# Optimization experiments

Measured on AMD Instinct MI355X. Metric: run time of the kernel, lower is better.

Reference implementation:

```python
import jax, jax.numpy as jnp
import numpy as np

EMB = 512
H = 8
DK = EMB // H          # 64
MAX_SEQ = 768
TOPK = MAX_SEQ // 2    # 384


def setup_inputs() -> dict:
    key = jax.random.key(0)
    ks = jax.random.split(key, 16)
    B, S, E = 1, MAX_SEQ, EMB

    def w(k, shape):
        return jax.random.normal(k, shape, dtype=jnp.float32) * 0.02

    return {
        "x": jax.random.normal(ks[0], (B, S, E), dtype=jnp.float32),
        # main attention projections (Linear weights stored as (in, out))
        "Wq": w(ks[1], (E, E)), "bq": w(ks[2], (E,)),
        "Wk": w(ks[3], (E, E)), "bk": w(ks[4], (E,)),
        "Wv": w(ks[5], (E, E)), "bv": w(ks[6], (E,)),
        "Wo": w(ks[7], (E, E)), "bo": w(ks[8], (E,)),
        # indexer projections: wq -> (E, H*DK)=(E,E), wk -> (E, DK), weights_proj -> (E, H)
        "iq_W": w(ks[9], (E, H * DK)), "iq_b": w(ks[10], (H * DK,)),
        "ik_W": w(ks[11], (E, DK)),    "ik_b": w(ks[12], (DK,)),
        "wp_W": w(ks[13], (E, H)),     "wp_b": w(ks[14], (H,)),
    }


def reference(x, Wq, bq, Wk, bk, Wv, bv, Wo, bo, iq_W, iq_b, ik_W, ik_b, wp_W, wp_b):
    B, S, E = x.shape
    scaling = 1.0 / np.sqrt(DK)

    def split_heads(z):  # (B,S,E) -> (B,H,S,DK)
        return z.reshape(B, S, H, DK).transpose(0, 2, 1, 3)

    Q = split_heads(x @ Wq + bq)
    K = split_heads(x @ Wk + bk)
    V = split_heads(x @ Wv + bv)

    # --- indexer: per-token relevance scores ---
    q_idx = (x @ iq_W + iq_b).reshape(B, S, H, DK).transpose(0, 2, 1, 3)  # (B,H,S,DK)
    k_idx = x @ ik_W + ik_b                                               # (B,S,DK)
    w_idx = x @ wp_W + wp_b                                               # (B,S,H)
    score = jax.nn.relu(jnp.einsum('bhsd,btd->bhst', q_idx, k_idx))       # (B,H,S,S)
    indexer_score = jnp.einsum('bhst,bsh->bst', score, w_idx)             # (B,S,S)

    # --- top-k selection (set-equivalent to argpartition in the original) ---
    topk_idx = jax.lax.top_k(indexer_score, TOPK)[1]                      # (B,S,TOPK) int32

    # --- gather sparse K/V per query token ---
    def gather_b(Zb, idxb):  # Zb:(H,S,DK), idxb:(S,TOPK) -> (H,S,TOPK,DK)
        return Zb[:, idxb, :]
    K_s = jax.vmap(gather_b)(K, topk_idx)  # (B,H,S,TOPK,DK)
    V_s = jax.vmap(gather_b)(V, topk_idx)  # (B,H,S,TOPK,DK)

    # --- sparse attention over selected tokens ---
    sc = jnp.einsum('bhsd,bhskd->bhsk', Q, K_s) * scaling  # (B,H,S,TOPK)
    wts = jax.nn.softmax(sc, axis=-1)
    attn = jnp.einsum('bhsk,bhskd->bhsd', wts, V_s)        # (B,H,S,DK)

    out = attn.transpose(0, 2, 1, 3).reshape(B, S, E) @ Wo + bo
    return out
```

## Files before the change

### kernel.cpp

```cpp
#include <hip/hip_runtime.h>
#include <hip/hip_bf16.h>
#include <math.h>

#define S 768
#define E 512
#define H 8
#define DK 64
#define TOPK 384

typedef short bf16x8 __attribute__((ext_vector_type(8)));
typedef float f32x4 __attribute__((ext_vector_type(4)));

__device__ __forceinline__ unsigned short f2bf(float x) {
  unsigned u = __float_as_uint(x);
  unsigned r = u + 0x7FFFu + ((u >> 16) & 1u);
  return (unsigned short)(r >> 16);
}
__device__ __forceinline__ float bf2f(unsigned short h) {
  return __uint_as_float(((unsigned)h) << 16);
}
__device__ __forceinline__ void split1(float x, unsigned short& h, unsigned short& l) {
  h = f2bf(x);
  l = f2bf(x - bf2f(h));
}

__device__ __forceinline__ void mfma3(f32x4& d, bf16x8 ah, bf16x8 al,
                                      bf16x8 bh, bf16x8 bl) {
  d = __builtin_amdgcn_mfma_f32_16x16x32_bf16(ah, bh, d, 0, 0, 0);
  d = __builtin_amdgcn_mfma_f32_16x16x32_bf16(ah, bl, d, 0, 0, 0);
  d = __builtin_amdgcn_mfma_f32_16x16x32_bf16(al, bh, d, 0, 0, 0);
}
__device__ __forceinline__ void mfma2(f32x4& d, bf16x8 ah, bf16x8 al, bf16x8 bh) {
  d = __builtin_amdgcn_mfma_f32_16x16x32_bf16(ah, bh, d, 0, 0, 0);
  d = __builtin_amdgcn_mfma_f32_16x16x32_bf16(al, bh, d, 0, 0, 0);
}

__device__ __forceinline__ bf16x8 ldfrag(const unsigned short* p) {
  return *reinterpret_cast<const bf16x8*>(p);
}

struct PrepTab {
  const float* src[8];
  unsigned short* hi[8];
  unsigned short* lo[8];
};

__global__ __launch_bounds__(256) void prep_kernel(PrepTab t) {
  const int seg = blockIdx.z;
  const int rows = (seg == 0) ? 768 : 512;
  const int cols = (seg == 5) ? 64 : ((seg == 6) ? 8 : 512);
  const int tx = (seg == 6) ? 2 : ((cols + 31) >> 5);
  const int ty = rows >> 5;
  if ((int)blockIdx.x >= tx || (int)blockIdx.y >= ty) return;
  const int r0 = blockIdx.y * 32, c0 = blockIdx.x * 32;
  const int tid = threadIdx.x;
  const int rl = tid >> 3, c4 = (tid & 7) << 2;
  const float* src = t.src[seg];
  if (seg == 0) {
    float4 v = *(const float4*)(src + (size_t)(r0 + rl) * cols + c0 + c4);
    unsigned short h[4], l[4];
    split1(v.x, h[0], l[0]); split1(v.y, h[1], l[1]);
    split1(v.z, h[2], l[2]); split1(v.w, h[3], l[3]);
    size_t off = (size_t)(r0 + rl) * cols + c0 + c4;
    *(ushort4*)(t.hi[seg] + off) = make_ushort4(h[0], h[1], h[2], h[3]);
    *(ushort4*)(t.lo[seg] + off) = make_ushort4(l[0], l[1], l[2], l[3]);
  } else {
    __shared__ float ts[32][33];
    #pragma unroll
    for (int j = 0; j < 4; ++j) {
      int c = c4 + j;
      ts[rl][c] = (c0 + c < cols) ? src[(size_t)(r0 + rl) * cols + c0 + c] : 0.0f;
    }
    __syncthreads();
    float v0 = ts[c4 + 0][rl], v1 = ts[c4 + 1][rl];
    float v2 = ts[c4 + 2][rl], v3 = ts[c4 + 3][rl];
    unsigned short h[4], l[4];
    split1(v0, h[0], l[0]); split1(v1, h[1], l[1]);
    split1(v2, h[2], l[2]); split1(v3, h[3], l[3]);
    size_t off = (size_t)(c0 + rl) * 512 + r0 + c4;
    *(ushort4*)(t.hi[seg] + off) = make_ushort4(h[0], h[1], h[2], h[3]);
    *(ushort4*)(t.lo[seg] + off) = make_ushort4(l[0], l[1], l[2], l[3]);
  }
}

struct ProjTab {
  const unsigned short* whi[6];
  const unsigned short* wlo[6];
  const float* bias[6];
};

__global__ __launch_bounds__(256) void proj_mfma_kernel(
    const unsigned short* __restrict__ Xhi, const unsigned short* __restrict__ Xlo,
    ProjTab pt,
    unsigned short* __restrict__ Qhi, unsigned short* __restrict__ Qlo,
    unsigned short* __restrict__ Khi, unsigned short* __restrict__ Klo,
    unsigned short* __restrict__ VThi,
    unsigned short* __restrict__ QIhi, unsigned short* __restrict__ QIlo,
    unsigned short* __restrict__ KIhi, unsigned short* __restrict__ KIlo,
    float* __restrict__ WI) {
  __shared__ __align__(16) unsigned short Ah[64][72];
  __shared__ __align__(16) unsigned short Al[64][72];
  __shared__ __align__(16) unsigned short Bh[64][72];
  __shared__ __align__(16) unsigned short Bl[64][72];
  const int bx = blockIdx.x;
  int seg, nt;
  if (bx < 32) { seg = bx >> 3; nt = bx & 7; }
  else         { seg = 4 + (bx - 32); nt = 0; }
  const int m0 = blockIdx.y * 64;
  const int n0 = nt * 64;
  const int tid = threadIdx.x;
  const int lane = tid & 63;
  const int wave = tid >> 6;
  const int mq = (wave >> 1) << 5;
  const int nq = (wave & 1) << 5;
  const int l15 = lane & 15;
  const int q8 = (lane >> 4) << 3;
  const int q4 = (lane >> 4) << 2;
  const unsigned short* Whi = pt.whi[seg];
  const unsigned short* Wlo = pt.wlo[seg];

  f32x4 acc[2][2] = {};
  for (int cc = 0; cc < 8; ++cc) {
    const int k0 = cc << 6;
    #pragma unroll
    for (int j = 0; j < 2; ++j) {
      const int flat = tid + (j << 8);
      const int mm = flat >> 3;
      const int kc = (flat & 7) << 3;
      const size_t ga = (size_t)(m0 + mm) * 512 + k0 + kc;
      const size_t gb = (size_t)(n0 + mm) * 512 + k0 + kc;
      *(bf16x8*)&Ah[mm][kc] = ldfrag(Xhi + ga);
      *(bf16x8*)&Al[mm][kc] = ldfrag(Xlo + ga);
      *(bf16x8*)&Bh[mm][kc] = ldfrag(Whi + gb);
      *(bf16x8*)&Bl[mm][kc] = ldfrag(Wlo + gb);
    }
    __syncthreads();
    #pragma unroll
    for (int ki = 0; ki < 64; ki += 32) {
      const int kk = ki + q8;
      bf16x8 ah0 = *(const bf16x8*)&Ah[mq + l15][kk];
      bf16x8 al0 = *(const bf16x8*)&Al[mq + l15][kk];
      bf16x8 ah1 = *(const bf16x8*)&Ah[mq + 16 + l15][kk];
      bf16x8 al1 = *(const bf16x8*)&Al[mq + 16 + l15][kk];
      bf16x8 bh0 = *(const bf16x8*)&Bh[nq + l15][kk];
      bf16x8 bl0 = *(const bf16x8*)&Bl[nq + l15][kk];
      bf16x8 bh1 = *(const bf16x8*)&Bh[nq + 16 + l15][kk];
      bf16x8 bl1 = *(const bf16x8*)&Bl[nq + 16 + l15][kk];
      mfma3(acc[0][0], ah0, al0, bh0, bl0);
      mfma3(acc[0][1], ah0, al0, bh1, bl1);
      mfma3(acc[1][0], ah1, al1, bh0, bl0);
      mfma3(acc[1][1], ah1, al1, bh1, bl1);
    }
    __syncthreads();
  }

  const float* bias = pt.bias[seg];
  #pragma unroll
  for (int ntt = 0; ntt < 2; ++ntt) {
    const int nloc = n0 + nq + ntt * 16 + l15;
    const float bv = (seg == 5 && nloc >= 8) ? 0.0f : bias[nloc];
    #pragma unroll
    for (int mt = 0; mt < 2; ++mt) {
      #pragma unroll
      for (int r = 0; r < 4; ++r) {
        const int m = m0 + mq + mt * 16 + q4 + r;
        const float v = acc[mt][ntt][r] + bv;
        unsigned short h16, l16;
        if (seg == 0) {
          split1(v, h16, l16);
          Qhi[(size_t)m * 512 + nloc] = h16;
          Qlo[(size_t)m * 512 + nloc] = l16;
        } else if (seg == 1) {
          const int hh = nloc >> 6, dd = nloc & 63;
          split1(v, h16, l16);
          Khi[((size_t)hh * S + m) * 64 + dd] = h16;
          Klo[((size_t)hh * S + m) * 64 + dd] = l16;
        } else if (seg == 2) {
          VThi[((size_t)(nloc >> 6) * 64 + (nloc & 63)) * S + m] = f2bf(v);
        } else if (seg == 3) {
          split1(v, h16, l16);
          QIhi[(size_t)m * 512 + nloc] = h16;
          QIlo[(size_t)m * 512 + nloc] = l16;
        } else if (seg == 4) {
          split1(v, h16, l16);
          KIhi[(size_t)m * 64 + nloc] = h16;
          KIlo[(size_t)m * 64 + nloc] = l16;
        } else {
          if (nloc < 8) WI[(size_t)m * 8 + nloc] = v;
        }
      }
    }
  }
}

__global__ __launch_bounds__(512) void indexer_mfma_kernel(
    const unsigned short* __restrict__ QIhi, const unsigned short* __restrict__ QIlo,
    const unsigned short* __restrict__ KIhi, const unsigned short* __restrict__ KIlo,
    const float* __restrict__ WI, float* __restrict__ ISC) {
  __shared__ float wis[32][8];
  __shared__ float AccL[32][65];
  const int s0 = blockIdx.y * 32, t0 = blockIdx.x * 64;
  const int tid512 = threadIdx.x;
  const int z = tid512 >> 8;
  const int tid = tid512 & 255;
  const int lane = tid & 63;
  const int wave = tid >> 6;
  const int mq = (wave >> 1) << 4;
  const int nqb = (wave & 1) << 5;
  const int l15 = lane & 15;
  const int q8 = (lane >> 4) << 3;
  const int q4 = (lane >> 4) << 2;
  if (tid512 < 256) wis[tid512 >> 3][tid512 & 7] = WI[(size_t)(s0 + (tid512 >> 3)) * 8 + (tid512 & 7)];
  __syncthreads();

  const size_t arow = (size_t)(s0 + mq + l15) * 512;
  const size_t brow0 = (size_t)(t0 + nqb + l15) * 64;
  const size_t brow1 = (size_t)(t0 + nqb + 16 + l15) * 64;

  bf16x8 kfh[2][2], kfl[2][2];
  #pragma unroll
  for (int kk = 0; kk < 2; ++kk) {
    const int kb = kk * 32 + q8;
    kfh[kk][0] = ldfrag(KIhi + brow0 + kb);
    kfl[kk][0] = ldfrag(KIlo + brow0 + kb);
    kfh[kk][1] = ldfrag(KIhi + brow1 + kb);
    kfl[kk][1] = ldfrag(KIlo + brow1 + kb);
  }

  float accI[2][4] = {};
  #pragma unroll
  for (int hh = 0; hh < 4; ++hh) {
    const int h = z * 4 + hh;
    f32x4 d[2] = {};
    #pragma unroll
    for (int kk = 0; kk < 2; ++kk) {
      const int ka = h * 64 + kk * 32 + q8;
      bf16x8 ah = ldfrag(QIhi + arow + ka);
      bf16x8 al = ldfrag(QIlo + arow + ka);
      mfma3(d[0], ah, al, kfh[kk][0], kfl[kk][0]);
      mfma3(d[1], ah, al, kfh[kk][1], kfl[kk][1]);
    }
    #pragma unroll
    for (int r = 0; r < 4; ++r) {
      const float w = wis[mq + q4 + r][h];
      accI[0][r] = fmaf(fmaxf(d[0][r], 0.0f), w, accI[0][r]);
      accI[1][r] = fmaf(fmaxf(d[1][r], 0.0f), w, accI[1][r]);
    }
  }
  if (z == 1) {
    #pragma unroll
    for (int ntt = 0; ntt < 2; ++ntt)
      #pragma unroll
      for (int r = 0; r < 4; ++r)
        AccL[mq + q4 + r][nqb + ntt * 16 + l15] = accI[ntt][r];
  }
  __syncthreads();
  if (z == 0) {
    #pragma unroll
    for (int ntt = 0; ntt < 2; ++ntt)
      #pragma unroll
      for (int r = 0; r < 4; ++r)
        ISC[(size_t)(s0 + mq + q4 + r) * S + t0 + nqb + ntt * 16 + l15] =
            accI[ntt][r] + AccL[mq + q4 + r][nqb + ntt * 16 + l15];
  }
}

__global__ __launch_bounds__(256) void topk_kernel(
    const float* __restrict__ ISC, unsigned* __restrict__ Mask,
    float* __restrict__ Sum, float* __restrict__ ATTacc) {
  __shared__ unsigned ordv[768];
  __shared__ int hist[256];
  __shared__ int gsum[16];
  __shared__ int sc[256];
  __shared__ unsigned mw[24];
  __shared__ unsigned sh_prefix;
  __shared__ int sh_R;
  const int s = blockIdx.x;
  const int tid = threadIdx.x;
  for (int i = tid; i < 768; i += 256) {
    float f = ISC[s * 768 + i] + 0.0f;
    unsigned u = __float_as_uint(f);
    ordv[i] = (u & 0x80000000u) ? ~u : (u | 0x80000000u);
  }
  {
    const float4 z4 = {0.0f, 0.0f, 0.0f, 0.0f};
    if (tid < 128) *(float4*)(ATTacc + (size_t)s * 512 + tid * 4) = z4;
  }
  if (tid < 24) mw[tid] = 0u;
  if (tid < H) Sum[tid * S + s] = 0.0f;
  if (tid == 0) { sh_prefix = 0u; sh_R = TOPK; }
  __syncthreads();
  for (int pass = 0; pass < 4; ++pass) {
    const int shift = 24 - pass * 8;
    hist[tid] = 0;
    __syncthreads();
    const unsigned pm = (pass == 0) ? 0u : (0xFFFFFFFFu << (shift + 8));
    const unsigned pref = sh_prefix;
    for (int i = tid; i < 768; i += 256) {
      unsigned o = ordv[i];
      if ((o & pm) == pref) atomicAdd(&hist[(o >> shift) & 255], 1);
    }
    __syncthreads();
    if (tid < 16) {
      int t = 0;
      #pragma unroll
      for (int k = 0; k < 16; ++k) t += hist[tid * 16 + k];
      gsum[tid] = t;
    }
    __syncthreads();
    if (tid == 0) {
      int R = sh_R;
      int G = 0;
      int g = 15;
      for (; g > 0; --g) {
        if (G + gsum[g] >= R) break;
        G += gsum[g];
      }
      int b = 15;
      for (; b > 0; --b) {
        int c = hist[g * 16 + b];
        if (G + c >= R) break;
        G += c;
      }
      sh_prefix = sh_prefix | ((unsigned)(g * 16 + b) << shift);
      sh_R = R - G;
    }
    __syncthreads();
  }
  const unsigned thr = sh_prefix;
  const int need_eq = sh_R;
  const int base = tid * 3;
  unsigned o0 = ordv[base], o1 = ordv[base + 1], o2 = ordv[base + 2];
  int c = (o0 == thr) + (o1 == thr) + (o2 == thr);
  sc[tid] = c;
  __syncthreads();
  for (int off = 1; off < 256; off <<= 1) {
    int v = (tid >= off) ? sc[tid - off] : 0;
    __syncthreads();
    sc[tid] += v;
    __syncthreads();
  }
  int rank = sc[tid] - c;
  if (o0 > thr || (o0 == thr && rank < need_eq))
    atomicOr(&mw[base >> 5], 1u << (base & 31));
  if (o0 == thr) ++rank;
  if (o1 > thr || (o1 == thr && rank < need_eq))
    atomicOr(&mw[(base + 1) >> 5], 1u << ((base + 1) & 31));
  if (o1 == thr) ++rank;
  if (o2 > thr || (o2 == thr && rank < need_eq))
    atomicOr(&mw[(base + 2) >> 5], 1u << ((base + 2) & 31));
  __syncthreads();
  if (tid < 24) Mask[s * 24 + tid] = mw[tid];
}

__global__ __launch_bounds__(256) void sattn_kernel(
    const unsigned short* __restrict__ Qhi, const unsigned short* __restrict__ Qlo,
    const unsigned short* __restrict__ Khi, const unsigned short* __restrict__ Klo,
    const unsigned short* __restrict__ VThi,
    const unsigned* __restrict__ Mask, float* __restrict__ ATTacc,
    float* __restrict__ Sum) {
  __shared__ __align__(16) unsigned short Pshi[32][40];
  __shared__ __align__(16) unsigned short Pslo[32][40];
  __shared__ unsigned msk[32][6];
  __shared__ float rsumf[32];
  const int ks = blockIdx.x;
  const int s0 = blockIdx.y * 32;
  const int h  = blockIdx.z;
  const int tid = threadIdx.x;
  const int lane = tid & 63;
  const int wave = tid >> 6;
  const int l15 = lane & 15;
  const int q8 = (lane >> 4) << 3;
  const int q4 = (lane >> 4) << 2;
  const int mq = (wave >> 1) << 4;
  const int nq = (wave & 1) << 4;
  const int db = (wave & 1) << 5;

  if (tid < 192) msk[tid & 31][tid >> 5] = Mask[(size_t)(s0 + (tid & 31)) * 24 + ks * 6 + (tid >> 5)];
  if (tid < 32) rsumf[tid] = 0.0f;
  __syncthreads();

  const size_t qrow = (size_t)(s0 + mq + l15) * 512 + h * 64;
  bf16x8 qh0 = ldfrag(Qhi + qrow + 0 + q8);
  bf16x8 ql0 = ldfrag(Qlo + qrow + 0 + q8);
  bf16x8 qh1 = ldfrag(Qhi + qrow + 32 + q8);
  bf16x8 ql1 = ldfrag(Qlo + qrow + 32 + q8);

  f32x4 oacc[2] = {};
  for (int ct = 0; ct < 6; ++ct) {
    const int tch = ks * 192 + ct * 32;
    f32x4 d = {0.0f, 0.0f, 0.0f, 0.0f};
    const size_t krow = ((size_t)h * S + tch + nq + l15) * 64;
    {
      bf16x8 bh0 = ldfrag(Khi + krow + 0 + q8);
      bf16x8 bl0 = ldfrag(Klo + krow + 0 + q8);
      bf16x8 bh1 = ldfrag(Khi + krow + 32 + q8);
      bf16x8 bl1 = ldfrag(Klo + krow + 32 + q8);
      mfma3(d, qh0, ql0, bh0, bl0);
      mfma3(d, qh1, ql1, bh1, bl1);
    }
    const int tl = ct * 32 + nq + l15;
    float e[4];
    #pragma unroll
    for (int r = 0; r < 4; ++r) {
      const int srow = mq + q4 + r;
      const unsigned w = msk[srow][tl >> 5];
      e[r] = ((w >> (tl & 31)) & 1u) ? __expf(d[r] * 0.125f) : 0.0f;
      unsigned short h16, l16;
      split1(e[r], h16, l16);
      Pshi[srow][nq + l15] = h16;
      Pslo[srow][nq + l15] = l16;
    }
    float v0 = e[0], v1 = e[1], v2 = e[2], v3 = e[3];
    #pragma unroll
    for (int off = 1; off < 16; off <<= 1) {
      v0 += __shfl_xor(v0, off);
      v1 += __shfl_xor(v1, off);
      v2 += __shfl_xor(v2, off);
      v3 += __shfl_xor(v3, off);
    }
    if (l15 == 0) {
      atomicAdd(&rsumf[mq + q4 + 0], v0);
      atomicAdd(&rsumf[mq + q4 + 1], v1);
      atomicAdd(&rsumf[mq + q4 + 2], v2);
      atomicAdd(&rsumf[mq + q4 + 3], v3);
    }
    __syncthreads();
    bf16x8 pah = *(const bf16x8*)&Pshi[mq + l15][q8];
    bf16x8 pal = *(const bf16x8*)&Pslo[mq + l15][q8];
    #pragma unroll
    for (int dt = 0; dt < 2; ++dt) {
      const size_t vrow = ((size_t)h * 64 + db + dt * 16 + l15) * S + tch;
      bf16x8 vbh = ldfrag(VThi + vrow + q8);
      mfma2(oacc[dt], pah, pal, vbh);
    }
    __syncthreads();
  }
  #pragma unroll
  for (int dt = 0; dt < 2; ++dt) {
    const int dd = db + dt * 16 + l15;
    #pragma unroll
    for (int r = 0; r < 4; ++r) {
      const int s = s0 + mq + q4 + r;
      atomicAdd(&ATTacc[(size_t)s * E + h * DK + dd], oacc[dt][r]);
    }
  }
  if (tid < 32) atomicAdd(&Sum[(size_t)h * S + s0 + tid], rsumf[tid]);
}

__global__ __launch_bounds__(512) void out_mfma_kernel(
    const float* __restrict__ ATTacc, const float* __restrict__ Sum,
    const unsigned short* __restrict__ WoThi,
    const float* __restrict__ bo, float* __restrict__ out) {
  __shared__ float AccL[16][65];
  __shared__ float ivs[16][8];
  const int tid512 = threadIdx.x;
  const int wave8 = tid512 >> 6;
  const int z = wave8 >> 2;
  const int wave = wave8 & 3;
  const int lane = tid512 & 63;
  const int m0 = blockIdx.y * 16;
  const int n0 = blockIdx.x * 64 + wave * 16;
  const int l15 = lane & 15;
  const int q8 = (lane >> 4) << 3;
  const int q4 = (lane >> 4) << 2;
  if (tid512 < 128) {
    const int r = tid512 >> 3, hh = tid512 & 7;
    ivs[r][hh] = 1.0f / Sum[(size_t)hh * S + m0 + r];
  }
  __syncthreads();
  const size_t arow = (size_t)(m0 + l15) * 512;
  const size_t brow = (size_t)(n0 + l15) * 512;
  int ko = (z << 8) + q8;
  bf16x8 cah, cal;
  {
    const float inv0 = ivs[l15][(ko >> 6) & 7];
    float4 a = *(const float4*)(ATTacc + arow + ko);
    float4 b = *(const float4*)(ATTacc + arow + ko + 4);
    float v[8] = {a.x, a.y, a.z, a.w, b.x, b.y, b.z, b.w};
    #pragma unroll
    for (int i = 0; i < 8; ++i) {
      unsigned short hh, ll;
      split1(v[i] * inv0, hh, ll);
      cah[i] = (short)hh; cal[i] = (short)ll;
    }
  }
  bf16x8 cbh = ldfrag(WoThi + brow + ko);
  f32x4 acc = {};
  #pragma unroll
  for (int it = 0; it < 8; ++it) {
    const int kn = ko + 32;
    float4 na = *(const float4*)(ATTacc + arow + kn);
    float4 nb = *(const float4*)(ATTacc + arow + kn + 4);
    bf16x8 nbh = ldfrag(WoThi + brow + kn);
    mfma2(acc, cah, cal, cbh);
    const float invn = ivs[l15][(kn >> 6) & 7];
    float v[8] = {na.x, na.y, na.z, na.w, nb.x, nb.y, nb.z, nb.w};
    #pragma unroll
    for (int i = 0; i < 8; ++i) {
      unsigned short hh, ll;
      split1(v[i] * invn, hh, ll);
      cah[i] = (short)hh; cal[i] = (short)ll;
    }
    cbh = nbh;
    ko = kn;
  }
  if (z == 1) {
    #pragma unroll
    for (int r = 0; r < 4; ++r)
      AccL[q4 + r][wave * 16 + l15] = acc[r];
  }
  __syncthreads();
  if (z == 0) {
    const int n = n0 + l15;
    const float bv = bo[n];
    #pragma unroll
    for (int r = 0; r < 4; ++r)
      out[(size_t)(m0 + q4 + r) * 512 + n] =
          acc[r] + AccL[q4 + r][wave * 16 + l15] + bv;
  }
}

extern "C" void kernel_launch(void* const* d_in, const int* in_sizes, int n_in,
                              void* d_out, int out_size, void* d_ws, size_t ws_size,
                              hipStream_t stream) {
  const float* x    = (const float*)d_in[0];
  const float* Wq   = (const float*)d_in[1];
  const float* bq   = (const float*)d_in[2];
  const float* Wk   = (const float*)d_in[3];
  const float* bk   = (const float*)d_in[4];
  const float* Wv   = (const float*)d_in[5];
  const float* bv   = (const float*)d_in[6];
  const float* Wo   = (const float*)d_in[7];
  const float* bo   = (const float*)d_in[8];
  const float* iqW  = (const float*)d_in[9];
  const float* iqb  = (const float*)d_in[10];
  const float* ikW  = (const float*)d_in[11];
  const float* ikb  = (const float*)d_in[12];
  const float* wpW  = (const float*)d_in[13];
  const float* wpb  = (const float*)d_in[14];

  float* ws = (float*)d_ws;
  float* WI   = ws;
  float* ISC  = WI + S * H;
  unsigned* Mask = (unsigned*)(ISC + S * S);
  float* Sum  = (float*)(Mask + S * 24);
  float* ATTacc = Sum + H * S;
  unsigned short* u = (unsigned short*)(ATTacc + S * E);
  unsigned short* Xhi  = u;             u += S * E;
  unsigned short* Xlo  = u;             u += S * E;
  unsigned short* Qhi  = u;             u += S * E;
  unsigned short* Qlo  = u;             u += S * E;
  unsigned short* Khi  = u;             u += S * E;
  unsigned short* Klo  = u;             u += S * E;
  unsigned short* VThi = u;             u += S * E;
  unsigned short* QIhi = u;             u += S * E;
  unsigned short* QIlo = u;             u += S * E;
  unsigned short* KIhi = u;             u += S * DK;
  unsigned short* KIlo = u;             u += S * DK;
  unsigned short* WTq_hi = u;           u += E * E;
  unsigned short* WTk_hi = u;           u += E * E;
  unsigned short* WTv_hi = u;           u += E * E;
  unsigned short* WTiq_hi = u;          u += E * E;
  unsigned short* WTik_hi = u;          u += 64 * E;
  unsigned short* WTwp_hi = u;          u += 64 * E;
  unsigned short* WTo_hi = u;           u += E * E;
  unsigned short* WTq_lo = u;           u += E * E;
  unsigned short* WTk_lo = u;           u += E * E;
  unsigned short* WTv_lo = u;           u += E * E;
  unsigned short* WTiq_lo = u;          u += E * E;
  unsigned short* WTik_lo = u;          u += 64 * E;
  unsigned short* WTwp_lo = u;          u += 64 * E;
  unsigned short* WTo_lo = u;           u += E * E;

  PrepTab prep;
  prep.src[0] = x;    prep.hi[0] = Xhi;     prep.lo[0] = Xlo;
  prep.src[1] = Wq;   prep.hi[1] = WTq_hi;  prep.lo[1] = WTq_lo;
  prep.src[2] = Wk;   prep.hi[2] = WTk_hi;  prep.lo[2] = WTk_lo;
  prep.src[3] = Wv;   prep.hi[3] = WTv_hi;  prep.lo[3] = WTv_lo;
  prep.src[4] = iqW;  prep.hi[4] = WTiq_hi; prep.lo[4] = WTiq_lo;
  prep.src[5] = ikW;  prep.hi[5] = WTik_hi; prep.lo[5] = WTik_lo;
  prep.src[6] = wpW;  prep.hi[6] = WTwp_hi; prep.lo[6] = WTwp_lo;
  prep.src[7] = Wo;   prep.hi[7] = WTo_hi;  prep.lo[7] = WTo_lo;

  ProjTab pt;
  pt.whi[0] = WTq_hi;  pt.wlo[0] = WTq_lo;  pt.bias[0] = bq;
  pt.whi[1] = WTk_hi;  pt.wlo[1] = WTk_lo;  pt.bias[1] = bk;
  pt.whi[2] = WTv_hi;  pt.wlo[2] = WTv_lo;  pt.bias[2] = bv;
  pt.whi[3] = WTiq_hi; pt.wlo[3] = WTiq_lo; pt.bias[3] = iqb;
  pt.whi[4] = WTik_hi; pt.wlo[4] = WTik_lo; pt.bias[4] = ikb;
  pt.whi[5] = WTwp_hi; pt.wlo[5] = WTwp_lo; pt.bias[5] = wpb;

  prep_kernel<<<dim3(16, 24, 8), dim3(256), 0, stream>>>(prep);
  proj_mfma_kernel<<<dim3(34, S / 64), dim3(256), 0, stream>>>(
      Xhi, Xlo, pt, Qhi, Qlo, Khi, Klo, VThi, QIhi, QIlo, KIhi, KIlo, WI);
  indexer_mfma_kernel<<<dim3(S / 64, S / 32), dim3(512), 0, stream>>>(
      QIhi, QIlo, KIhi, KIlo, WI, ISC);
  topk_kernel<<<dim3(S), dim3(256), 0, stream>>>(ISC, Mask, Sum, ATTacc);
  sattn_kernel<<<dim3(4, S / 32, H), dim3(256), 0, stream>>>(
      Qhi, Qlo, Khi, Klo, VThi, Mask, ATTacc, Sum);
  out_mfma_kernel<<<dim3(8, 48), dim3(512), 0, stream>>>(
      ATTacc, Sum, WTo_hi, bo, (float*)d_out);
}
```

Measured before the change: 157.2 us.

## Stage Q in LDS for indexer and share K/V tiles across 64-row sattn blocks

The indexer kernel drops its two-group head split and 512-thread cross-group reduction. It now uses 256 threads that loop over head pairs and cooperatively stage the QI hi/lo slices into shared memory before the MFMAs. The sparse attention kernel doubles its query tile to 64 rows with 512 threads. Each K/V chunk is loaded once into LDS and shared by all eight waves, replacing per-wave global fragment loads. This cuts redundant global/L2 traffic, at the cost of extra barriers per chunk, fewer blocks, and more LDS per block.

```diff
diff --git a/kernel.cpp b/kernel.cpp
--- a/kernel.cpp
+++ b/kernel.cpp
@@ -193,16 +193,15 @@
   }
 }
 
-__global__ __launch_bounds__(512) void indexer_mfma_kernel(
+__global__ __launch_bounds__(256) void indexer_mfma_kernel(
     const unsigned short* __restrict__ QIhi, const unsigned short* __restrict__ QIlo,
     const unsigned short* __restrict__ KIhi, const unsigned short* __restrict__ KIlo,
     const float* __restrict__ WI, float* __restrict__ ISC) {
+  __shared__ __align__(16) unsigned short Qh[32][136];
+  __shared__ __align__(16) unsigned short Ql[32][136];
   __shared__ float wis[32][8];
-  __shared__ float AccL[32][65];
   const int s0 = blockIdx.y * 32, t0 = blockIdx.x * 64;
-  const int tid512 = threadIdx.x;
-  const int z = tid512 >> 8;
-  const int tid = tid512 & 255;
+  const int tid = threadIdx.x;
   const int lane = tid & 63;
   const int wave = tid >> 6;
   const int mq = (wave >> 1) << 4;
@@ -210,13 +209,10 @@
   const int l15 = lane & 15;
   const int q8 = (lane >> 4) << 3;
   const int q4 = (lane >> 4) << 2;
-  if (tid512 < 256) wis[tid512 >> 3][tid512 & 7] = WI[(size_t)(s0 + (tid512 >> 3)) * 8 + (tid512 & 7)];
-  __syncthreads();
-
-  const size_t arow = (size_t)(s0 + mq + l15) * 512;
+  wis[tid >> 3][tid & 7] = WI[(size_t)(s0 + (tid >> 3)) * 8 + (tid & 7)];
+
   const size_t brow0 = (size_t)(t0 + nqb + l15) * 64;
   const size_t brow1 = (size_t)(t0 + nqb + 16 + l15) * 64;
-
   bf16x8 kfh[2][2], kfl[2][2];
   #pragma unroll
   for (int kk = 0; kk < 2; ++kk) {
@@ -227,42 +223,44 @@
     kfl[kk][1] = ldfrag(KIlo + brow1 + kb);
   }
 
+  const int smm = tid >> 3;
+  const int skc = (tid & 7) << 4;
   float accI[2][4] = {};
+  for (int hp = 0; hp < 4; ++hp) {
+    __syncthreads();
+    {
+      const size_t g = (size_t)(s0 + smm) * 512 + hp * 128 + skc;
+      *(bf16x8*)&Qh[smm][skc]     = ldfrag(QIhi + g);
+      *(bf16x8*)&Qh[smm][skc + 8] = ldfrag(QIhi + g + 8);
+      *(bf16x8*)&Ql[smm][skc]     = ldfrag(QIlo + g);
+      *(bf16x8*)&Ql[smm][skc + 8] = ldfrag(QIlo + g + 8);
+    }
+    __syncthreads();
+    #pragma unroll
+    for (int hh = 0; hh < 2; ++hh) {
+      const int h = hp * 2 + hh;
+      f32x4 d[2] = {};
+      #pragma unroll
+      for (int kk = 0; kk < 2; ++kk) {
+        const int ka = hh * 64 + kk * 32 + q8;
+        bf16x8 ah = *(const bf16x8*)&Qh[mq + l15][ka];
+        bf16x8 al = *(const bf16x8*)&Ql[mq + l15][ka];
+        mfma3(d[0], ah, al, kfh[kk][0], kfl[kk][0]);
+        mfma3(d[1], ah, al, kfh[kk][1], kfl[kk][1]);
+      }
+      #pragma unroll
+      for (int r = 0; r < 4; ++r) {
+        const float w = wis[mq + q4 + r][h];
+        accI[0][r] = fmaf(fmaxf(d[0][r], 0.0f), w, accI[0][r]);
+        accI[1][r] = fmaf(fmaxf(d[1][r], 0.0f), w, accI[1][r]);
+      }
+    }
+  }
   #pragma unroll
-  for (int hh = 0; hh < 4; ++hh) {
-    const int h = z * 4 + hh;
-    f32x4 d[2] = {};
-    #pragma unroll
-    for (int kk = 0; kk < 2; ++kk) {
-      const int ka = h * 64 + kk * 32 + q8;
-      bf16x8 ah = ldfrag(QIhi + arow + ka);
-      bf16x8 al = ldfrag(QIlo + arow + ka);
-      mfma3(d[0], ah, al, kfh[kk][0], kfl[kk][0]);
-      mfma3(d[1], ah, al, kfh[kk][1], kfl[kk][1]);
-    }
-    #pragma unroll
-    for (int r = 0; r < 4; ++r) {
-      const float w = wis[mq + q4 + r][h];
-      accI[0][r] = fmaf(fmaxf(d[0][r], 0.0f), w, accI[0][r]);
-      accI[1][r] = fmaf(fmaxf(d[1][r], 0.0f), w, accI[1][r]);
-    }
-  }
-  if (z == 1) {
-    #pragma unroll
-    for (int ntt = 0; ntt < 2; ++ntt)
-      #pragma unroll
-      for (int r = 0; r < 4; ++r)
-        AccL[mq + q4 + r][nqb + ntt * 16 + l15] = accI[ntt][r];
-  }
-  __syncthreads();
-  if (z == 0) {
-    #pragma unroll
-    for (int ntt = 0; ntt < 2; ++ntt)
-      #pragma unroll
-      for (int r = 0; r < 4; ++r)
-        ISC[(size_t)(s0 + mq + q4 + r) * S + t0 + nqb + ntt * 16 + l15] =
-            accI[ntt][r] + AccL[mq + q4 + r][nqb + ntt * 16 + l15];
-  }
+  for (int ntt = 0; ntt < 2; ++ntt)
+    #pragma unroll
+    for (int r = 0; r < 4; ++r)
+      ISC[(size_t)(s0 + mq + q4 + r) * S + t0 + nqb + ntt * 16 + l15] = accI[ntt][r];
 }
 
 __global__ __launch_bounds__(256) void topk_kernel(
@@ -353,18 +351,21 @@
   if (tid < 24) Mask[s * 24 + tid] = mw[tid];
 }
 
-__global__ __launch_bounds__(256) void sattn_kernel(
+__global__ __launch_bounds__(512) void sattn_kernel(
     const unsigned short* __restrict__ Qhi, const unsigned short* __restrict__ Qlo,
     const unsigned short* __restrict__ Khi, const unsigned short* __restrict__ Klo,
     const unsigned short* __restrict__ VThi,
     const unsigned* __restrict__ Mask, float* __restrict__ ATTacc,
     float* __restrict__ Sum) {
-  __shared__ __align__(16) unsigned short Pshi[32][40];
-  __shared__ __align__(16) unsigned short Pslo[32][40];
-  __shared__ unsigned msk[32][6];
-  __shared__ float rsumf[32];
+  __shared__ __align__(16) unsigned short Pshi[64][40];
+  __shared__ __align__(16) unsigned short Pslo[64][40];
+  __shared__ __align__(16) unsigned short Ksh[32][72];
+  __shared__ __align__(16) unsigned short Ksl[32][72];
+  __shared__ __align__(16) unsigned short Vsh[64][40];
+  __shared__ unsigned msk[64][6];
+  __shared__ float rsumf[64];
   const int ks = blockIdx.x;
-  const int s0 = blockIdx.y * 32;
+  const int s0 = blockIdx.y * 64;
   const int h  = blockIdx.z;
   const int tid = threadIdx.x;
   const int lane = tid & 63;
@@ -376,9 +377,9 @@
   const int nq = (wave & 1) << 4;
   const int db = (wave & 1) << 5;
 
-  if (tid < 192) msk[tid & 31][tid >> 5] = Mask[(size_t)(s0 + (tid & 31)) * 24 + ks * 6 + (tid >> 5)];
-  if (tid < 32) rsumf[tid] = 0.0f;
-  __syncthreads();
+  if (tid < 384) msk[tid & 63][tid >> 6] =
+      Mask[(size_t)(s0 + (tid & 63)) * 24 + ks * 6 + (tid >> 6)];
+  if (tid < 64) rsumf[tid] = 0.0f;
 
   const size_t qrow = (size_t)(s0 + mq + l15) * 512 + h * 64;
   bf16x8 qh0 = ldfrag(Qhi + qrow + 0 + q8);
@@ -386,16 +387,30 @@
   bf16x8 qh1 = ldfrag(Qhi + qrow + 32 + q8);
   bf16x8 ql1 = ldfrag(Qlo + qrow + 32 + q8);
 
+  const int t2 = tid & 255;
   f32x4 oacc[2] = {};
   for (int ct = 0; ct < 6; ++ct) {
     const int tch = ks * 192 + ct * 32;
+    __syncthreads();
+    if (tid < 256) {
+      const int tr = t2 >> 3;
+      const int kc = (t2 & 7) << 3;
+      const size_t gk = ((size_t)h * S + tch + tr) * 64 + kc;
+      *(bf16x8*)&Ksh[tr][kc] = ldfrag(Khi + gk);
+      *(bf16x8*)&Ksl[tr][kc] = ldfrag(Klo + gk);
+    } else {
+      const int vr = t2 >> 2;
+      const int tc = (t2 & 3) << 3;
+      *(bf16x8*)&Vsh[vr][tc] =
+          ldfrag(VThi + ((size_t)h * 64 + vr) * S + tch + tc);
+    }
+    __syncthreads();
     f32x4 d = {0.0f, 0.0f, 0.0f, 0.0f};
-    const size_t krow = ((size_t)h * S + tch + nq + l15) * 64;
     {
-      bf16x8 bh0 = ldfrag(Khi + krow + 0 + q8);
-      bf16x8 bl0 = ldfrag(Klo + krow + 0 + q8);
-      bf16x8 bh1 = ldfrag(Khi + krow + 32 + q8);
-      bf16x8 bl1 = ldfrag(Klo + krow + 32 + q8);
+      bf16x8 bh0 = *(const bf16x8*)&Ksh[nq + l15][q8];
+      bf16x8 bl0 = *(const bf16x8*)&Ksl[nq + l15][q8];
+      bf16x8 bh1 = *(const bf16x8*)&Ksh[nq + l15][32 + q8];
+      bf16x8 bl1 = *(const bf16x8*)&Ksl[nq + l15][32 + q8];
       mfma3(d, qh0, ql0, bh0, bl0);
       mfma3(d, qh1, ql1, bh1, bl1);
     }
@@ -430,11 +445,9 @@
     bf16x8 pal = *(const bf16x8*)&Pslo[mq + l15][q8];
     #pragma unroll
     for (int dt = 0; dt < 2; ++dt) {
-      const size_t vrow = ((size_t)h * 64 + db + dt * 16 + l15) * S + tch;
-      bf16x8 vbh = ldfrag(VThi + vrow + q8);
+      bf16x8 vbh = *(const bf16x8*)&Vsh[db + dt * 16 + l15][q8];
       mfma2(oacc[dt], pah, pal, vbh);
     }
-    __syncthreads();
   }
   #pragma unroll
   for (int dt = 0; dt < 2; ++dt) {
@@ -445,7 +458,8 @@
       atomicAdd(&ATTacc[(size_t)s * E + h * DK + dd], oacc[dt][r]);
     }
   }
-  if (tid < 32) atomicAdd(&Sum[(size_t)h * S + s0 + tid], rsumf[tid]);
+  __syncthreads();
+  if (tid < 64) atomicAdd(&Sum[(size_t)h * S + s0 + tid], rsumf[tid]);
 }
 
 __global__ __launch_bounds__(512) void out_mfma_kernel(
@@ -594,10 +608,10 @@
   prep_kernel<<<dim3(16, 24, 8), dim3(256), 0, stream>>>(prep);
   proj_mfma_kernel<<<dim3(34, S / 64), dim3(256), 0, stream>>>(
       Xhi, Xlo, pt, Qhi, Qlo, Khi, Klo, VThi, QIhi, QIlo, KIhi, KIlo, WI);
-  indexer_mfma_kernel<<<dim3(S / 64, S / 32), dim3(512), 0, stream>>>(
+  indexer_mfma_kernel<<<dim3(S / 64, S / 32), dim3(256), 0, stream>>>(
       QIhi, QIlo, KIhi, KIlo, WI, ISC);
   topk_kernel<<<dim3(S), dim3(256), 0, stream>>>(ISC, Mask, Sum, ATTacc);
-  sattn_kernel<<<dim3(4, S / 32, H), dim3(256), 0, stream>>>(
+  sattn_kernel<<<dim3(4, S / 64, H), dim3(512), 0, stream>>>(
       Qhi, Qlo, Khi, Klo, VThi, Mask, ATTacc, Sum);
   out_mfma_kernel<<<dim3(8, 48), dim3(512), 0, stream>>>(
       ATTacc, Sum, WTo_hi, bo, (float*)d_out);
```

Result: faster. 151.2 us (-3.8%).
